# Kernel tuning notes

Measured on AMD Instinct MI355X. Metric: run time of the kernel, lower is better.

The kernel has to match this reference:

```python
import jax, jax.numpy as jnp
import numpy as np

B, U, HEADS, S = 16, 1024, 8, 1024


def setup_inputs() -> dict:
    key = jax.random.key(0)
    k1, k2, k3, k4 = jax.random.split(key, 4)
    x = jax.random.normal(k1, (B, U, S), dtype=jnp.float32)
    mask = jax.random.randint(k2, (B, S, S), 0, 2).astype(bool)
    w_qkv = jax.random.normal(k3, (3 * U, U), dtype=jnp.float32) * 0.02
    w_out = jax.random.normal(k4, (U, U), dtype=jnp.float32) * 0.02
    return {"x": x, "mask": mask, "w_qkv": w_qkv, "w_out": w_out}


def reference(x, mask, w_qkv, w_out):
    # x: (B, U, S), mask: (B, n_queries, n_keys) bool
    b, u, s = x.shape
    h = HEADS
    c = u // h  # head (chunk) size
    scale = 1.0 / np.sqrt(c).astype(np.float32)

    # 1x1-conv QKV projection (bias=False): (3U, U) x (B, U, S) -> (B, 3U, S)
    qkv = jnp.einsum('ou,bus->bos', w_qkv, x)
    Q, K, V = jnp.split(qkv, 3, axis=1)           # each (B, U, S)
    Qh = Q.reshape(b, h, c, s)
    Kh = K.reshape(b, h, c, s)
    Vh = V.reshape(b, h, c, s)

    # attention logits: (B, H, n_q, n_k)
    A = jnp.einsum('bhcq,bhck->bhqk', Qh, Kh)

    # relu activation with per-query valid-key-count normalization
    m = mask.sum(axis=2)[:, :, None]              # (B, n_q, 1) count of valid keys
    n_elem = jnp.where(mask, m, 1).astype(A.dtype)[:, None]  # (B, 1, n_q, n_k)
    mask_b = mask[:, None]                        # broadcast over heads
    A = jnp.where(mask_b, jax.nn.relu(A) * scale, -jnp.inf)
    A = A / n_elem
    A = jnp.where(jnp.isinf(A), jnp.zeros((), A.dtype), A)

    # attention-value aggregation (faithful math of broadcast+sum): (B, H, C, n_q)
    Ch = jnp.einsum('bhqk,bhck->bhcq', A, Vh)
    Cc = Ch.reshape(b, u, s)

    # finishing 1x1-conv linear layer
    return jnp.einsum('ou,bus->bos', w_out, Cc)
```

## Files before the change

### kernel.cpp

```cpp
#include <hip/hip_runtime.h>

#define B_DIM 16
#define U_DIM 1024
#define H_DIM 8
#define S_DIM 1024
#define C_DIM 128
#define KD 1024
#define SCALE 0.08838834764831845f

typedef __attribute__((ext_vector_type(8))) short s16x8;
typedef __attribute__((ext_vector_type(4))) float f32x4;

__device__ __forceinline__ void gll16(const void* g, void* l) {
  __builtin_amdgcn_global_load_lds(
      (const __attribute__((address_space(1))) unsigned int*)g,
      (__attribute__((address_space(3))) unsigned int*)l, 16, 0, 0);
}
__device__ __forceinline__ unsigned short f2bf(float f) {
  unsigned u = __float_as_uint(f);
  u += 0x7FFF + ((u >> 16) & 1u);
  return (unsigned short)(u >> 16);
}
#define MFMA16(a, b, c) __builtin_amdgcn_mfma_f32_16x16x32_bf16(a, b, c, 0, 0, 0)

__global__ void detect_mask(const unsigned char* __restrict__ mask_raw, int* __restrict__ flag) {
  __shared__ int not01, notf;
  if (threadIdx.x == 0) { not01 = 0; notf = 0; }
  __syncthreads();
  const unsigned int* p = (const unsigned int*)mask_raw;
  int l01 = 0, lf = 0;
  for (int i = threadIdx.x; i < 4096; i += 256) {
    unsigned int v = p[i];
    if (v != 0u && v != 1u) l01 = 1;
    if (v != 0u && v != 0x3F800000u) lf = 1;
  }
  if (l01) atomicOr(&not01, 1);
  if (lf) atomicOr(&notf, 1);
  __syncthreads();
  if (threadIdx.x == 0) flag[0] = (!not01) ? 0 : ((!notf) ? 2 : 1);
}

__global__ __launch_bounds__(256) void pack_mask(const unsigned char* __restrict__ mask_raw,
                                                 const int* __restrict__ flag,
                                                 unsigned long long* __restrict__ bits) {
  __shared__ unsigned char tile[64][80];
  const int t = threadIdx.x;
  const int kt = blockIdx.x * 64, qw = blockIdx.y, b = blockIdx.z;
  const int mk = flag[0];
  const int q = t >> 2, kbase = (t & 3) * 16;
  const size_t row = (size_t)(b * S_DIM + qw * 64 + q);
  if (mk == 1) {
    uint4 v = *(const uint4*)(mask_raw + (row << 10) + kt + kbase);
    *(uint4*)&tile[q][kbase] = v;
  } else if (mk == 0) {
    const int* p = (const int*)mask_raw + (row << 10) + kt + kbase;
#pragma unroll
    for (int j = 0; j < 4; ++j) {
      int4 v = ((const int4*)p)[j];
      uchar4 o;
      o.x = v.x ? 1 : 0; o.y = v.y ? 1 : 0; o.z = v.z ? 1 : 0; o.w = v.w ? 1 : 0;
      *(uchar4*)&tile[q][kbase + j * 4] = o;
    }
  } else {
    const float* p = (const float*)mask_raw + (row << 10) + kt + kbase;
#pragma unroll
    for (int j = 0; j < 4; ++j) {
      float4 v = ((const float4*)p)[j];
      uchar4 o;
      o.x = (v.x != 0.f) ? 1 : 0; o.y = (v.y != 0.f) ? 1 : 0;
      o.z = (v.z != 0.f) ? 1 : 0; o.w = (v.w != 0.f) ? 1 : 0;
      *(uchar4*)&tile[q][kbase + j * 4] = o;
    }
  }
  __syncthreads();
  const int wave = t >> 6, lane = t & 63;
#pragma unroll
  for (int qq = 0; qq < 16; ++qq) {
    int qr = wave * 16 + qq;
    unsigned long long bal = __ballot(tile[qr][lane] != 0);
    if (lane == 0)
      bits[(size_t)blockIdx.x * (B_DIM * S_DIM) + (size_t)b * S_DIM + qw * 64 + qr] = bal;
  }
}

__global__ __launch_bounds__(256) void invm_from_bits(const unsigned long long* __restrict__ bits,
                                                      float* __restrict__ invm) {
  int idx = blockIdx.x * 256 + threadIdx.x;
  int s = 0;
#pragma unroll
  for (int kt = 0; kt < S_DIM / 64; ++kt)
    s += __popcll(bits[(size_t)kt * (B_DIM * S_DIM) + idx]);
  invm[idx] = (s > 0) ? (SCALE / (float)s) : 0.f;
}

__global__ __launch_bounds__(256) void cvt_bf16(const float* __restrict__ in,
                                                unsigned short* __restrict__ out, int n) {
  int i = (blockIdx.x * 256 + threadIdx.x) * 4;
  if (i < n) {
    float4 v = *(const float4*)(in + i);
    ushort4 o;
    o.x = f2bf(v.x); o.y = f2bf(v.y); o.z = f2bf(v.z); o.w = f2bf(v.w);
    *(ushort4*)(out + i) = o;
  }
}

__global__ __launch_bounds__(256) void transpose_x(const float* __restrict__ x,
                                                   unsigned short* __restrict__ xT) {
  __shared__ float T[32][33];
  const int t = threadIdx.x, r = t >> 3, c4 = (t & 7) * 4;
  const int s0 = blockIdx.x * 32, u0 = blockIdx.y * 32;
  const size_t base = (size_t)blockIdx.z * U_DIM * S_DIM;
  float4 v = *(const float4*)(x + base + (size_t)(u0 + r) * S_DIM + s0 + c4);
  T[r][c4 + 0] = v.x; T[r][c4 + 1] = v.y; T[r][c4 + 2] = v.z; T[r][c4 + 3] = v.w;
  __syncthreads();
  ushort4 o;
  o.x = f2bf(T[c4 + 0][r]); o.y = f2bf(T[c4 + 1][r]);
  o.z = f2bf(T[c4 + 2][r]); o.w = f2bf(T[c4 + 3][r]);
  *(ushort4*)(xT + base + (size_t)(s0 + r) * U_DIM + u0 + c4) = o;
}

__global__ __launch_bounds__(256) void transpose_v(const unsigned short* __restrict__ qkvT,
                                                   unsigned short* __restrict__ VT) {
  __shared__ unsigned short T[32][34];
  const int t = threadIdx.x, r = t >> 3, c4 = (t & 7) * 4;
  const int k0 = blockIdx.x * 32, c0 = blockIdx.y * 32;
  const unsigned short* qb = qkvT + (size_t)blockIdx.z * S_DIM * (3 * U_DIM);
  ushort4 v = *(const ushort4*)(qb + (size_t)(k0 + r) * (3 * U_DIM) + 2 * U_DIM + c0 + c4);
  T[r][c4 + 0] = v.x; T[r][c4 + 1] = v.y; T[r][c4 + 2] = v.z; T[r][c4 + 3] = v.w;
  __syncthreads();
  ushort4 o;
  o.x = T[c4 + 0][r]; o.y = T[c4 + 1][r]; o.z = T[c4 + 2][r]; o.w = T[c4 + 3][r];
  *(ushort4*)(VT + (size_t)blockIdx.z * U_DIM * S_DIM + (size_t)(c0 + r) * S_DIM + k0 + c4) = o;
}

template <typename OUT>
__global__ __launch_bounds__(512, 2) void gemm256(const unsigned short* __restrict__ A,
                                                  const unsigned short* __restrict__ Bm,
                                                  OUT* __restrict__ D,
                                                  long long sAb, long long sBb, long long sDb,
                                                  int N) {
  __shared__ unsigned short sA0[256 * 64], sB0[256 * 64];
  __shared__ unsigned short sA1[256 * 64], sB1[256 * 64];
  const int tid = threadIdx.x;
  const int wave = tid >> 6, lane = tid & 63;
  const int l15 = lane & 15, quad = lane >> 4;
  const int wm = wave & 3, wn = wave >> 2;
  const unsigned int Lb = blockIdx.x + gridDim.x * (blockIdx.y + gridDim.y * blockIdx.z);
  const unsigned int nwg = gridDim.x * gridDim.y * gridDim.z;
  const unsigned int logical = (Lb & 7u) * (nwg >> 3) + (Lb >> 3);
  const int bx = logical % gridDim.x;
  const unsigned int rem = logical / gridDim.x;
  const int by = rem % gridDim.y;
  const int bz = rem / gridDim.y;
  const int m0 = by * 256, n0 = bx * 256;
  A += (size_t)bz * sAb + (size_t)m0 * KD;
  Bm += (size_t)bz * sBb + (size_t)n0 * KD;
  D += (size_t)bz * sDb;

  const int r0 = tid >> 3;
  const int kc0 = (tid & 7) ^ (r0 & 7);
  const unsigned short* pA = A + (size_t)r0 * KD + kc0 * 8;
  const unsigned short* pB = Bm + (size_t)r0 * KD + kc0 * 8;
  const int wo = wave * 512;

#define STG_U0(SA, K0)                                        \
  do {                                                        \
    gll16(pA + (K0), &(SA)[wo]);                              \
    gll16(pA + 64 * KD + (K0), &(SA)[4096 + wo]);             \
  } while (0)
#define STG_U1(SA, K0)                                        \
  do {                                                        \
    gll16(pA + 128 * KD + (K0), &(SA)[8192 + wo]);            \
    gll16(pA + 192 * KD + (K0), &(SA)[12288 + wo]);           \
  } while (0)
#define STG_U2(SB, K0)                                        \
  do {                                                        \
    gll16(pB + (K0), &(SB)[wo]);                              \
    gll16(pB + 128 * KD + (K0), &(SB)[8192 + wo]);            \
  } while (0)
#define STG_U3(SB, K0)                                        \
  do {                                                        \
    gll16(pB + 64 * KD + (K0), &(SB)[4096 + wo]);             \
    gll16(pB + 192 * KD + (K0), &(SB)[12288 + wo]);           \
  } while (0)

#define WAITB(VN)                                             \
  do {                                                        \
    asm volatile("s_waitcnt vmcnt(" #VN ")" ::: "memory");    \
    __builtin_amdgcn_s_barrier();                             \
    asm volatile("" ::: "memory");                            \
  } while (0)

  s16x8 a[4][2];
  f32x4 acc[4][8] = {};

#define LDA(SA)                                                                         \
  do {                                                                                  \
    _Pragma("unroll") for (int i = 0; i < 4; ++i) {                                     \
      int row = wm * 64 + i * 16 + l15;                                                 \
      _Pragma("unroll") for (int ks = 0; ks < 2; ++ks)                                  \
          a[i][ks] = *(const s16x8*)&(SA)[row * 64 + (((ks * 4 + quad) ^ (row & 7)) * 8)]; \
    }                                                                                   \
  } while (0)

#define PHASE(SB, P)                                                                    \
  do {                                                                                  \
    s16x8 b[2][2];                                                                      \
    _Pragma("unroll") for (int jj = 0; jj < 2; ++jj) {                                  \
      int row = wn * 128 + ((P) * 2 + jj) * 16 + l15;                                   \
      _Pragma("unroll") for (int ks = 0; ks < 2; ++ks)                                  \
          b[jj][ks] = *(const s16x8*)&(SB)[row * 64 + (((ks * 4 + quad) ^ (row & 7)) * 8)]; \
    }                                                                                   \
    __builtin_amdgcn_s_setprio(1);                                                      \
    _Pragma("unroll") for (int ks = 0; ks < 2; ++ks)                                    \
        _Pragma("unroll") for (int i = 0; i < 4; ++i)                                   \
            _Pragma("unroll") for (int jj = 0; jj < 2; ++jj)                            \
                acc[i][(P) * 2 + jj] = MFMA16(a[i][ks], b[jj][ks], acc[i][(P) * 2 + jj]); \
    __builtin_amdgcn_s_setprio(0);                                                      \
  } while (0)

#define TILE(SA, SB, SAn, SBn, K1)                            \
  do {                                                        \
    WAITB(2);                                                 \
    STG_U0(SAn, K1);                                          \
    LDA(SA);                                                  \
    PHASE(SB, 0);                                             \
    STG_U1(SAn, K1);                                          \
    PHASE(SB, 1);                                             \
    WAITB(4);                                                 \
    STG_U2(SBn, K1);                                          \
    PHASE(SB, 2);                                             \
    STG_U3(SBn, K1);                                          \
    PHASE(SB, 3);                                             \
  } while (0)

  STG_U0(sA0, 0); STG_U1(sA0, 0); STG_U2(sB0, 0); STG_U3(sB0, 0);

  for (int kt = 0; kt < 14; kt += 2) {
    TILE(sA0, sB0, sA1, sB1, (kt + 1) * 64);
    TILE(sA1, sB1, sA0, sB0, (kt + 2) * 64);
  }
  TILE(sA0, sB0, sA1, sB1, 15 * 64);

  {
    WAITB(2);
    LDA(sA1);
    PHASE(sB1, 0);
    PHASE(sB1, 1);
    WAITB(0);
    PHASE(sB1, 2);
    PHASE(sB1, 3);
  }
#undef TILE
#undef PHASE
#undef LDA
#undef WAITB
#undef STG_U0
#undef STG_U1
#undef STG_U2
#undef STG_U3

#pragma unroll
  for (int i = 0; i < 4; ++i)
#pragma unroll
    for (int j = 0; j < 8; ++j) {
      f32x4 v = acc[i][j];
#pragma unroll
      for (int r = 0; r < 4; ++r) {
        int m = m0 + wm * 64 + i * 16 + quad * 4 + r;
        int n = n0 + wn * 128 + j * 16 + l15;
        if constexpr (sizeof(OUT) == 2) D[(size_t)m * N + n] = f2bf(v[r]);
        else D[(size_t)m * N + n] = v[r];
      }
    }
}

__global__ __launch_bounds__(256, 2) void attn_mfma(const unsigned short* __restrict__ qkvT,
                                                    const unsigned short* __restrict__ VT,
                                                    const unsigned long long* __restrict__ bits,
                                                    const float* __restrict__ invm,
                                                    unsigned short* __restrict__ CcT, int b0) {
  __shared__ unsigned short QV[64 * 128];
  __shared__ unsigned short Ks[64 * 128];
  __shared__ unsigned short Vs[128 * 64];
  __shared__ unsigned short Ps[64 * 64];
  __shared__ float invs[64];

  const int tid = threadIdx.x, wave = tid >> 6, lane = tid & 63;
  const int l15 = lane & 15, quad = lane >> 4;
  const int L = blockIdx.x + 16 * (blockIdx.y + 8 * blockIdx.z);
  const int cpx = (16 * H_DIM * gridDim.z) >> 3;
  const int logical = (L & 7) * cpx + (L >> 3);
  const int qt = logical & 15, h = (logical >> 4) & 7, z = logical >> 7;
  const int q0 = qt * 64, b = b0 + z;
  const unsigned short* qB = qkvT + (size_t)z * S_DIM * (3 * U_DIM);
  const unsigned short* Vb = VT + (size_t)z * U_DIM * S_DIM + (size_t)h * C_DIM * S_DIM;

#pragma unroll
  for (int t = 0; t < 4; ++t) {
    int p = wave * 256 + t * 64 + lane;
    int row = p >> 4, c = (p & 15) ^ (row & 7);
    gll16(qB + (size_t)(q0 + row) * (3 * U_DIM) + h * C_DIM + c * 8,
          &QV[(wave * 256 + t * 64) * 8]);
    gll16(qB + (size_t)(row) * (3 * U_DIM) + U_DIM + h * C_DIM + c * 8,
          &Ks[(wave * 256 + t * 64) * 8]);
    int vrow = p >> 3, vkc = (p & 7) ^ (vrow & 7);
    gll16(Vb + (size_t)vrow * S_DIM + vkc * 8, &Vs[(wave * 256 + t * 64) * 8]);
  }
  if (tid < 64) invs[tid] = invm[(size_t)b * S_DIM + q0 + tid];
  __syncthreads();

  s16x8 qf[4][4];
#pragma unroll
  for (int j = 0; j < 4; ++j)
#pragma unroll
    for (int kk = 0; kk < 4; ++kk) {
      int row = j * 16 + l15;
      qf[j][kk] = *(const s16x8*)&QV[row * 128 + ((kk * 4 + quad) ^ (row & 7)) * 8];
    }
  float invf[4];
#pragma unroll
  for (int j = 0; j < 4; ++j) invf[j] = invs[j * 16 + l15];

  f32x4 pacc[4][2] = {};

  for (int kt = 0; kt < S_DIM / 64; ++kt) {
    unsigned long long w64[4];
    {
      const unsigned long long* mw =
          bits + (size_t)kt * (B_DIM * S_DIM) + (size_t)b * S_DIM + q0;
#pragma unroll
      for (int j = 0; j < 4; ++j) w64[j] = mw[j * 16 + l15];
    }

    s16x8 af[4];
#pragma unroll
    for (int kk = 0; kk < 4; ++kk) {
      int row = wave * 16 + l15;
      af[kk] = *(const s16x8*)&Ks[row * 128 + ((kk * 4 + quad) ^ (row & 7)) * 8];
    }
    f32x4 sacc[4] = {};
    __builtin_amdgcn_s_setprio(1);
#pragma unroll
    for (int kk = 0; kk < 4; ++kk)
#pragma unroll
      for (int j = 0; j < 4; ++j) sacc[j] = MFMA16(af[kk], qf[j][kk], sacc[j]);
    __builtin_amdgcn_s_setprio(0);

#pragma unroll
    for (int j = 0; j < 4; ++j) {
      const unsigned int m4 = (unsigned int)(w64[j] >> (wave * 16 + quad * 4)) & 0xFu;
      float p[4];
#pragma unroll
      for (int r = 0; r < 4; ++r) {
        float t = fmaxf(sacc[j][r], 0.f) * invf[j];
        p[r] = ((m4 >> r) & 1u) ? t : 0.f;
      }
      unsigned int pk0, pk1;
      asm("v_cvt_pk_bf16_f32 %0, %1, %2" : "=v"(pk0) : "v"(p[0]), "v"(p[1]));
      asm("v_cvt_pk_bf16_f32 %0, %1, %2" : "=v"(pk1) : "v"(p[2]), "v"(p[3]));
      int q = j * 16 + l15;
      int chunk = (wave * 2 + (quad >> 1)) ^ (q & 7);
      *(uint2*)&Ps[q * 64 + chunk * 8 + (quad & 1) * 4] = make_uint2(pk0, pk1);
    }
    __syncthreads();

    if (kt < S_DIM / 64 - 1) {
      const int kn = (kt + 1) * 64;
      unsigned short* vdst = (kt & 1) ? Vs : QV;
#pragma unroll
      for (int t = 0; t < 4; ++t) {
        int p = wave * 256 + t * 64 + lane;
        int row = p >> 4, c = (p & 15) ^ (row & 7);
        gll16(qB + (size_t)(kn + row) * (3 * U_DIM) + U_DIM + h * C_DIM + c * 8,
              &Ks[(wave * 256 + t * 64) * 8]);
        int vrow = p >> 3, vkc = (p & 7) ^ (vrow & 7);
        gll16(Vb + (size_t)vrow * S_DIM + kn + vkc * 8, &vdst[(wave * 256 + t * 64) * 8]);
      }
    }

    const unsigned short* vbuf = (kt & 1) ? QV : Vs;
#pragma unroll
    for (int ks = 0; ks < 2; ++ks) {
      s16x8 pf[4], vf[2];
#pragma unroll
      for (int i = 0; i < 4; ++i) {
        int row = i * 16 + l15;
        pf[i] = *(const s16x8*)&Ps[row * 64 + ((ks * 4 + quad) ^ (row & 7)) * 8];
      }
#pragma unroll
      for (int j = 0; j < 2; ++j) {
        int row = wave * 32 + j * 16 + l15;
        vf[j] = *(const s16x8*)&vbuf[row * 64 + ((ks * 4 + quad) ^ (row & 7)) * 8];
      }
      __builtin_amdgcn_s_setprio(1);
#pragma unroll
      for (int i = 0; i < 4; ++i)
#pragma unroll
        for (int j = 0; j < 2; ++j) pacc[i][j] = MFMA16(pf[i], vf[j], pacc[i][j]);
      __builtin_amdgcn_s_setprio(0);
    }
    __syncthreads();
  }

  unsigned short* cb = CcT + (size_t)z * S_DIM * U_DIM;
#pragma unroll
  for (int i = 0; i < 4; ++i)
#pragma unroll
    for (int j = 0; j < 2; ++j) {
      f32x4 v = pacc[i][j];
#pragma unroll
      for (int r = 0; r < 4; ++r) {
        int q = q0 + i * 16 + quad * 4 + r;
        int c = h * C_DIM + wave * 32 + j * 16 + l15;
        cb[(size_t)q * U_DIM + c] = f2bf(v[r]);
      }
    }
}

extern "C" void kernel_launch(void* const* d_in, const int* in_sizes, int n_in,
                              void* d_out, int out_size, void* d_ws, size_t ws_size,
                              hipStream_t stream) {
  const float* x = (const float*)d_in[0];
  const unsigned char* mask_raw = (const unsigned char*)d_in[1];
  const float* w_qkv = (const float*)d_in[2];
  const float* w_out = (const float*)d_in[3];
  float* out = (float*)d_out;

  char* ws = (char*)d_ws;
  int* flag = (int*)ws;
  float* invm = (float*)(ws + 256);
  unsigned long long* bits = (unsigned long long*)(ws + 256 + 65536);
  unsigned short* wqkv_bf = (unsigned short*)((char*)bits + (size_t)B_DIM * S_DIM * 16 * 8);
  unsigned short* wout_bf = (unsigned short*)((char*)wqkv_bf + (size_t)3 * U_DIM * U_DIM * 2);
  char* heap = (char*)wout_bf + (size_t)U_DIM * U_DIM * 2;

  const size_t xT_pb = (size_t)U_DIM * S_DIM * 2;
  const size_t qkvT_pb = (size_t)3 * U_DIM * S_DIM * 2;
  const size_t vT_pb = (size_t)U_DIM * S_DIM * 2;
  const size_t ccT_pb = (size_t)U_DIM * S_DIM * 2;
  const size_t per_batch = xT_pb + qkvT_pb + vT_pb + ccT_pb;
  const size_t fixed = (size_t)(heap - ws);
  int nb = (ws_size > fixed) ? (int)((ws_size - fixed) / per_batch) : 1;
  if (nb < 1) nb = 1;
  if (nb > B_DIM) nb = B_DIM;

  unsigned short* xT = (unsigned short*)heap;
  unsigned short* qkvT = (unsigned short*)(heap + (size_t)nb * xT_pb);
  unsigned short* VT = (unsigned short*)(heap + (size_t)nb * (xT_pb + qkvT_pb));
  unsigned short* CcT = (unsigned short*)(heap + (size_t)nb * (xT_pb + qkvT_pb + vT_pb));

  detect_mask<<<1, 256, 0, stream>>>(mask_raw, flag);
  pack_mask<<<dim3(S_DIM / 64, S_DIM / 64, B_DIM), 256, 0, stream>>>(mask_raw, flag, bits);
  invm_from_bits<<<(B_DIM * S_DIM) / 256, 256, 0, stream>>>(bits, invm);
  cvt_bf16<<<(3 * U_DIM * U_DIM) / 1024, 256, 0, stream>>>(w_qkv, wqkv_bf, 3 * U_DIM * U_DIM);
  cvt_bf16<<<(U_DIM * U_DIM) / 1024, 256, 0, stream>>>(w_out, wout_bf, U_DIM * U_DIM);

  for (int b0 = 0; b0 < B_DIM; b0 += nb) {
    int cnt = (B_DIM - b0 < nb) ? (B_DIM - b0) : nb;
    transpose_x<<<dim3(S_DIM / 32, U_DIM / 32, cnt), 256, 0, stream>>>(
        x + (size_t)b0 * U_DIM * S_DIM, xT);
    gemm256<unsigned short><<<dim3(3 * U_DIM / 256, S_DIM / 256, cnt), 512, 0, stream>>>(
        xT, wqkv_bf, qkvT, (long long)U_DIM * S_DIM, 0LL, (long long)3 * U_DIM * S_DIM, 3 * U_DIM);
    transpose_v<<<dim3(S_DIM / 32, U_DIM / 32, cnt), 256, 0, stream>>>(qkvT, VT);
    attn_mfma<<<dim3(S_DIM / 64, H_DIM, cnt), 256, 0, stream>>>(
        qkvT, VT, bits, invm, CcT, b0);
    gemm256<float><<<dim3(S_DIM / 256, U_DIM / 256, cnt), 512, 0, stream>>>(
        wout_bf, CcT, out + (size_t)b0 * U_DIM * S_DIM, 0LL,
        (long long)U_DIM * S_DIM, (long long)U_DIM * S_DIM, S_DIM);
  }
}
```

Before: 462.0 us.

## Restructure GEMM main loop into barrier-separated phases with explicit schedule barriers

Reorganizes the double-buffered GEMM K-loop so that each phase issues its LDS reads and then passes a barrier, an lgkmcnt wait and sched_barrier fences before running its MFMAs, with a barrier after every phase. Global-to-LDS staging for the next tile is issued earlier, with A's two stages together up front, and the vmcnt waits are moved to the phase boundaries. The intent is to enforce a ping-pong style interleave of memory and MFMA work across waves and to stop the compiler from reordering them. The cost is more barriers per tile, which could add stall time.

```diff
diff --git a/kernel.cpp b/kernel.cpp
--- a/kernel.cpp
+++ b/kernel.cpp
@@ -184,14 +184,19 @@
     gll16(pB + 192 * KD + (K0), &(SB)[12288 + wo]);           \
   } while (0)
 
-#define WAITB(VN)                                             \
-  do {                                                        \
-    asm volatile("s_waitcnt vmcnt(" #VN ")" ::: "memory");    \
-    __builtin_amdgcn_s_barrier();                             \
-    asm volatile("" ::: "memory");                            \
+#define BARR() __builtin_amdgcn_s_barrier()
+#define SCHB() __builtin_amdgcn_sched_barrier(0)
+#define VMC(NN) asm volatile("s_waitcnt vmcnt(" #NN ")" ::: "memory")
+#define PH_ENTER()                                            \
+  do {                                                        \
+    SCHB();                                                   \
+    BARR();                                                   \
+    asm volatile("s_waitcnt lgkmcnt(0)" ::: "memory");        \
+    SCHB();                                                   \
   } while (0)
 
   s16x8 a[4][2];
+  s16x8 b[2][2];
   f32x4 acc[4][8] = {};
 
 #define LDA(SA)                                                                         \
@@ -203,58 +208,68 @@
     }                                                                                   \
   } while (0)
 
-#define PHASE(SB, P)                                                                    \
+#define DSRB(SB, P)                                                                     \
   do {                                                                                  \
-    s16x8 b[2][2];                                                                      \
     _Pragma("unroll") for (int jj = 0; jj < 2; ++jj) {                                  \
       int row = wn * 128 + ((P) * 2 + jj) * 16 + l15;                                   \
       _Pragma("unroll") for (int ks = 0; ks < 2; ++ks)                                  \
           b[jj][ks] = *(const s16x8*)&(SB)[row * 64 + (((ks * 4 + quad) ^ (row & 7)) * 8)]; \
     }                                                                                   \
+  } while (0)
+
+#define MM(P)                                                                           \
+  do {                                                                                  \
     __builtin_amdgcn_s_setprio(1);                                                      \
     _Pragma("unroll") for (int ks = 0; ks < 2; ++ks)                                    \
         _Pragma("unroll") for (int i = 0; i < 4; ++i)                                   \
             _Pragma("unroll") for (int jj = 0; jj < 2; ++jj)                            \
                 acc[i][(P) * 2 + jj] = MFMA16(a[i][ks], b[jj][ks], acc[i][(P) * 2 + jj]); \
     __builtin_amdgcn_s_setprio(0);                                                      \
-  } while (0)
-
-#define TILE(SA, SB, SAn, SBn, K1)                            \
-  do {                                                        \
-    WAITB(2);                                                 \
-    STG_U0(SAn, K1);                                          \
-    LDA(SA);                                                  \
-    PHASE(SB, 0);                                             \
-    STG_U1(SAn, K1);                                          \
-    PHASE(SB, 1);                                             \
-    WAITB(4);                                                 \
-    STG_U2(SBn, K1);                                          \
-    PHASE(SB, 2);                                             \
-    STG_U3(SBn, K1);                                          \
-    PHASE(SB, 3);                                             \
+    SCHB();                                                                             \
+  } while (0)
+
+#define TILE_ST(CA, CB, NA, NB, K1)                           \
+  do {                                                        \
+    STG_U0(NA, K1);                                           \
+    STG_U1(NA, K1);                                           \
+    LDA(CA);                                                  \
+    DSRB(CB, 0); PH_ENTER(); MM(0); BARR();                   \
+    STG_U2(NB, K1);                                           \
+    DSRB(CB, 1); SCHB(); VMC(6); PH_ENTER(); MM(1); BARR();   \
+    STG_U3(NB, K1);                                           \
+    DSRB(CB, 2); PH_ENTER(); MM(2); BARR();                   \
+    DSRB(CB, 3); SCHB(); VMC(2); PH_ENTER(); MM(3); BARR();   \
+  } while (0)
+
+#define TILE_LAST(CA, CB)                                     \
+  do {                                                        \
+    LDA(CA);                                                  \
+    DSRB(CB, 0); PH_ENTER(); MM(0); BARR();                   \
+    DSRB(CB, 1); SCHB(); VMC(0); PH_ENTER(); MM(1); BARR();   \
+    DSRB(CB, 2); PH_ENTER(); MM(2); BARR();                   \
+    DSRB(CB, 3); PH_ENTER(); MM(3);                           \
   } while (0)
 
   STG_U0(sA0, 0); STG_U1(sA0, 0); STG_U2(sB0, 0); STG_U3(sB0, 0);
+  VMC(2);
+  BARR();
 
   for (int kt = 0; kt < 14; kt += 2) {
-    TILE(sA0, sB0, sA1, sB1, (kt + 1) * 64);
-    TILE(sA1, sB1, sA0, sB0, (kt + 2) * 64);
-  }
-  TILE(sA0, sB0, sA1, sB1, 15 * 64);
-
-  {
-    WAITB(2);
-    LDA(sA1);
-    PHASE(sB1, 0);
-    PHASE(sB1, 1);
-    WAITB(0);
-    PHASE(sB1, 2);
-    PHASE(sB1, 3);
-  }
-#undef TILE
-#undef PHASE
+    TILE_ST(sA0, sB0, sA1, sB1, (kt + 1) * 64);
+    TILE_ST(sA1, sB1, sA0, sB0, (kt + 2) * 64);
+  }
+  TILE_ST(sA0, sB0, sA1, sB1, 15 * 64);
+  TILE_LAST(sA1, sB1);
+
+#undef TILE_ST
+#undef TILE_LAST
+#undef MM
+#undef DSRB
 #undef LDA
-#undef WAITB
+#undef PH_ENTER
+#undef VMC
+#undef SCHB
+#undef BARR
 #undef STG_U0
 #undef STG_U1
 #undef STG_U2
```

Measured after the change: 466.5 us. About the same (+1.0%).

## Double attention query tile to 128 with 8 waves sharing K/V tiles

Applied to the files above, without the earlier changes.

The attention kernel now processes 128 queries per block with 512 threads, so two wave groups share each staged K and V tile. This halves the global K/V traffic per query. The V prefetch for the next step is moved to the top of each iteration to overlap with the score MFMAs, while the K prefetch stays after the barrier. Inverse counts are now read directly from global memory instead of through shared memory. In exchange, LDS use per block roughly doubles and the grid has half as many blocks, which could lower occupancy. The GEMM tail is also refactored into a macro.

```diff
diff --git a/kernel.cpp b/kernel.cpp
--- a/kernel.cpp
+++ b/kernel.cpp
@@ -234,6 +234,17 @@
     PHASE(SB, 3);                                             \
   } while (0)
 
+#define TILE_LAST(CA, CB)                                     \
+  do {                                                        \
+    WAITB(2);                                                 \
+    LDA(CA);                                                  \
+    PHASE(CB, 0);                                             \
+    PHASE(CB, 1);                                             \
+    WAITB(0);                                                 \
+    PHASE(CB, 2);                                             \
+    PHASE(CB, 3);                                             \
+  } while (0)
+
   STG_U0(sA0, 0); STG_U1(sA0, 0); STG_U2(sB0, 0); STG_U3(sB0, 0);
 
   for (int kt = 0; kt < 14; kt += 2) {
@@ -241,17 +252,9 @@
     TILE(sA1, sB1, sA0, sB0, (kt + 2) * 64);
   }
   TILE(sA0, sB0, sA1, sB1, 15 * 64);
-
-  {
-    WAITB(2);
-    LDA(sA1);
-    PHASE(sB1, 0);
-    PHASE(sB1, 1);
-    WAITB(0);
-    PHASE(sB1, 2);
-    PHASE(sB1, 3);
-  }
+  TILE_LAST(sA1, sB1);
 #undef TILE
+#undef TILE_LAST
 #undef PHASE
 #undef LDA
 #undef WAITB
@@ -275,39 +278,41 @@
     }
 }
 
-__global__ __launch_bounds__(256, 2) void attn_mfma(const unsigned short* __restrict__ qkvT,
+__global__ __launch_bounds__(512, 2) void attn_mfma(const unsigned short* __restrict__ qkvT,
                                                     const unsigned short* __restrict__ VT,
                                                     const unsigned long long* __restrict__ bits,
                                                     const float* __restrict__ invm,
                                                     unsigned short* __restrict__ CcT, int b0) {
-  __shared__ unsigned short QV[64 * 128];
+  __shared__ unsigned short QV[128 * 128];
   __shared__ unsigned short Ks[64 * 128];
   __shared__ unsigned short Vs[128 * 64];
-  __shared__ unsigned short Ps[64 * 64];
-  __shared__ float invs[64];
+  __shared__ unsigned short Ps[128 * 64];
 
   const int tid = threadIdx.x, wave = tid >> 6, lane = tid & 63;
   const int l15 = lane & 15, quad = lane >> 4;
-  const int L = blockIdx.x + 16 * (blockIdx.y + 8 * blockIdx.z);
-  const int cpx = (16 * H_DIM * gridDim.z) >> 3;
+  const int qhalf = wave >> 2, kw = wave & 3;
+  const int L = blockIdx.x + 8 * (blockIdx.y + 8 * blockIdx.z);
+  const int cpx = (8 * H_DIM * gridDim.z) >> 3;
   const int logical = (L & 7) * cpx + (L >> 3);
-  const int qt = logical & 15, h = (logical >> 4) & 7, z = logical >> 7;
-  const int q0 = qt * 64, b = b0 + z;
+  const int qt = logical & 7, h = (logical >> 3) & 7, z = logical >> 6;
+  const int q0 = qt * 128, b = b0 + z;
   const unsigned short* qB = qkvT + (size_t)z * S_DIM * (3 * U_DIM);
   const unsigned short* Vb = VT + (size_t)z * U_DIM * S_DIM + (size_t)h * C_DIM * S_DIM;
 
 #pragma unroll
-  for (int t = 0; t < 4; ++t) {
-    int p = wave * 256 + t * 64 + lane;
+  for (int pp = 0; pp < 4; ++pp) {
+    int p = pp * 512 + tid;
     int row = p >> 4, c = (p & 15) ^ (row & 7);
-    gll16(qB + (size_t)(q0 + row) * (3 * U_DIM) + h * C_DIM + c * 8,
-          &QV[(wave * 256 + t * 64) * 8]);
-    gll16(qB + (size_t)(row) * (3 * U_DIM) + U_DIM + h * C_DIM + c * 8,
-          &Ks[(wave * 256 + t * 64) * 8]);
+    gll16(qB + (size_t)(q0 + row) * (3 * U_DIM) + h * C_DIM + c * 8, &QV[p * 8]);
+  }
+#pragma unroll
+  for (int pp = 0; pp < 2; ++pp) {
+    int p = pp * 512 + tid;
+    int row = p >> 4, c = (p & 15) ^ (row & 7);
+    gll16(qB + (size_t)row * (3 * U_DIM) + U_DIM + h * C_DIM + c * 8, &Ks[p * 8]);
     int vrow = p >> 3, vkc = (p & 7) ^ (vrow & 7);
-    gll16(Vb + (size_t)vrow * S_DIM + vkc * 8, &Vs[(wave * 256 + t * 64) * 8]);
-  }
-  if (tid < 64) invs[tid] = invm[(size_t)b * S_DIM + q0 + tid];
+    gll16(Vb + (size_t)vrow * S_DIM + vkc * 8, &Vs[p * 8]);
+  }
   __syncthreads();
 
   s16x8 qf[4][4];
@@ -315,20 +320,35 @@
   for (int j = 0; j < 4; ++j)
 #pragma unroll
     for (int kk = 0; kk < 4; ++kk) {
-      int row = j * 16 + l15;
+      int row = qhalf * 64 + j * 16 + l15;
       qf[j][kk] = *(const s16x8*)&QV[row * 128 + ((kk * 4 + quad) ^ (row & 7)) * 8];
     }
   float invf[4];
-#pragma unroll
-  for (int j = 0; j < 4; ++j) invf[j] = invs[j * 16 + l15];
+  {
+    const float* ivp = invm + (size_t)b * S_DIM + q0 + qhalf * 64;
+#pragma unroll
+    for (int j = 0; j < 4; ++j) invf[j] = ivp[j * 16 + l15];
+  }
+  __syncthreads();
 
   f32x4 pacc[4][2] = {};
 
   for (int kt = 0; kt < S_DIM / 64; ++kt) {
+    if (kt < S_DIM / 64 - 1) {
+      const int kn = (kt + 1) * 64;
+      unsigned short* vdst = (kt & 1) ? Vs : QV;
+#pragma unroll
+      for (int pp = 0; pp < 2; ++pp) {
+        int p = pp * 512 + tid;
+        int vrow = p >> 3, vkc = (p & 7) ^ (vrow & 7);
+        gll16(Vb + (size_t)vrow * S_DIM + kn + vkc * 8, &vdst[p * 8]);
+      }
+    }
+
     unsigned long long w64[4];
     {
       const unsigned long long* mw =
-          bits + (size_t)kt * (B_DIM * S_DIM) + (size_t)b * S_DIM + q0;
+          bits + (size_t)kt * (B_DIM * S_DIM) + (size_t)b * S_DIM + q0 + qhalf * 64;
 #pragma unroll
       for (int j = 0; j < 4; ++j) w64[j] = mw[j * 16 + l15];
     }
@@ -336,7 +356,7 @@
     s16x8 af[4];
 #pragma unroll
     for (int kk = 0; kk < 4; ++kk) {
-      int row = wave * 16 + l15;
+      int row = kw * 16 + l15;
       af[kk] = *(const s16x8*)&Ks[row * 128 + ((kk * 4 + quad) ^ (row & 7)) * 8];
     }
     f32x4 sacc[4] = {};
@@ -349,7 +369,7 @@
 
 #pragma unroll
     for (int j = 0; j < 4; ++j) {
-      const unsigned int m4 = (unsigned int)(w64[j] >> (wave * 16 + quad * 4)) & 0xFu;
+      const unsigned int m4 = (unsigned int)(w64[j] >> (kw * 16 + quad * 4)) & 0xFu;
       float p[4];
 #pragma unroll
       for (int r = 0; r < 4; ++r) {
@@ -359,23 +379,19 @@
       unsigned int pk0, pk1;
       asm("v_cvt_pk_bf16_f32 %0, %1, %2" : "=v"(pk0) : "v"(p[0]), "v"(p[1]));
       asm("v_cvt_pk_bf16_f32 %0, %1, %2" : "=v"(pk1) : "v"(p[2]), "v"(p[3]));
-      int q = j * 16 + l15;
-      int chunk = (wave * 2 + (quad >> 1)) ^ (q & 7);
+      int q = qhalf * 64 + j * 16 + l15;
+      int chunk = (kw * 2 + (quad >> 1)) ^ (q & 7);
       *(uint2*)&Ps[q * 64 + chunk * 8 + (quad & 1) * 4] = make_uint2(pk0, pk1);
     }
     __syncthreads();
 
     if (kt < S_DIM / 64 - 1) {
       const int kn = (kt + 1) * 64;
-      unsigned short* vdst = (kt & 1) ? Vs : QV;
-#pragma unroll
-      for (int t = 0; t < 4; ++t) {
-        int p = wave * 256 + t * 64 + lane;
+#pragma unroll
+      for (int pp = 0; pp < 2; ++pp) {
+        int p = pp * 512 + tid;
         int row = p >> 4, c = (p & 15) ^ (row & 7);
-        gll16(qB + (size_t)(kn + row) * (3 * U_DIM) + U_DIM + h * C_DIM + c * 8,
-              &Ks[(wave * 256 + t * 64) * 8]);
-        int vrow = p >> 3, vkc = (p & 7) ^ (vrow & 7);
-        gll16(Vb + (size_t)vrow * S_DIM + kn + vkc * 8, &vdst[(wave * 256 + t * 64) * 8]);
+        gll16(qB + (size_t)(kn + row) * (3 * U_DIM) + U_DIM + h * C_DIM + c * 8, &Ks[p * 8]);
       }
     }
 
@@ -385,12 +401,12 @@
       s16x8 pf[4], vf[2];
 #pragma unroll
       for (int i = 0; i < 4; ++i) {
-        int row = i * 16 + l15;
+        int row = qhalf * 64 + i * 16 + l15;
         pf[i] = *(const s16x8*)&Ps[row * 64 + ((ks * 4 + quad) ^ (row & 7)) * 8];
       }
 #pragma unroll
       for (int j = 0; j < 2; ++j) {
-        int row = wave * 32 + j * 16 + l15;
+        int row = kw * 32 + j * 16 + l15;
         vf[j] = *(const s16x8*)&vbuf[row * 64 + ((ks * 4 + quad) ^ (row & 7)) * 8];
       }
       __builtin_amdgcn_s_setprio(1);
@@ -411,8 +427,8 @@
       f32x4 v = pacc[i][j];
 #pragma unroll
       for (int r = 0; r < 4; ++r) {
-        int q = q0 + i * 16 + quad * 4 + r;
-        int c = h * C_DIM + wave * 32 + j * 16 + l15;
+        int q = q0 + qhalf * 64 + i * 16 + quad * 4 + r;
+        int c = h * C_DIM + kw * 32 + j * 16 + l15;
         cb[(size_t)q * U_DIM + c] = f2bf(v[r]);
       }
     }
@@ -463,7 +479,7 @@
     gemm256<unsigned short><<<dim3(3 * U_DIM / 256, S_DIM / 256, cnt), 512, 0, stream>>>(
         xT, wqkv_bf, qkvT, (long long)U_DIM * S_DIM, 0LL, (long long)3 * U_DIM * S_DIM, 3 * U_DIM);
     transpose_v<<<dim3(S_DIM / 32, U_DIM / 32, cnt), 256, 0, stream>>>(qkvT, VT);
-    attn_mfma<<<dim3(S_DIM / 64, H_DIM, cnt), 256, 0, stream>>>(
+    attn_mfma<<<dim3(S_DIM / 128, H_DIM, cnt), 512, 0, stream>>>(
         qkvT, VT, bits, invm, CcT, b0);
     gemm256<float><<<dim3(S_DIM / 256, U_DIM / 256, cnt), 512, 0, stream>>>(
         wout_bf, CcT, out + (size_t)b0 * U_DIM * S_DIM, 0LL,
```

Measured after the change: 462.8 us. Within noise of the previous version (+0.2%).
